# Kernel optimization log

Hardware: AMD Instinct MI355X
Metric: run time of the kernel (lower is better)

## Reference

```python
import jax, jax.numpy as jnp
import numpy as np

B, T, M, VM = 64, 512, 8, 50  # batch, time, num_modules, rois per module
EPS = 1e-5  # BatchNorm eps


def setup_inputs() -> dict:
    key = jax.random.key(0)
    ks = jax.random.split(key, 12)
    x = jax.random.normal(ks[0], (B, M * VM, T, 1), jnp.float32)
    # learned adjacency, torch init = ones/V; perturb slightly
    PA = jnp.full((M, VM, VM), 1.0 / VM, jnp.float32) + 0.01 * jax.random.normal(ks[1], (M, VM, VM), jnp.float32)
    conv_w = jax.random.normal(ks[2], (M,), jnp.float32)          # 1x1 conv weight (1->1 chan) per module
    conv_b = 0.1 * jax.random.normal(ks[3], (M,), jnp.float32)
    bn_gamma = 1.0 + 0.1 * jax.random.normal(ks[4], (M,), jnp.float32)
    bn_beta = 0.1 * jax.random.normal(ks[5], (M,), jnp.float32)
    bn_mean = 0.1 * jax.random.normal(ks[6], (M,), jnp.float32)
    bn_var = jax.random.uniform(ks[7], (M,), jnp.float32) + 0.5   # positive
    w1 = jax.random.normal(ks[8], (M, 8), jnp.float32) * 0.5      # Linear(1,8) weight per module
    b1 = 0.1 * jax.random.normal(ks[9], (M, 8), jnp.float32)
    w2 = jax.random.normal(ks[10], (M, 8), jnp.float32) * 0.5     # Linear(8,1) weight per module
    b2 = 0.1 * jax.random.normal(ks[11], (M,), jnp.float32)
    return dict(x=x, PA=PA, conv_w=conv_w, conv_b=conv_b, bn_gamma=bn_gamma, bn_beta=bn_beta,
                bn_mean=bn_mean, bn_var=bn_var, w1=w1, b1=b1, w2=w2, b2=b2)


def reference(x, PA, conv_w, conv_b, bn_gamma, bn_beta, bn_mean, bn_var, w1, b1, w2, b2):
    # x: [B, V_total, T, 1]; torch permute(0,3,2,1) -> [B, C=1, T, V_total]
    xp = x[..., 0].transpose(0, 2, 1)                 # [B, T, V_total]
    xm = xp.reshape(B, T, M, VM)                      # contiguous module blocks == index_select
    # UnitGCN: x_agg = x @ A per module
    agg = jnp.einsum('btmv,mvw->btmw', xm, PA)        # [B, T, M, VM]
    # 1x1 conv (scalar per module) + BatchNorm2d(1) in eval mode + ReLU
    y = agg * conv_w[:, None] + conv_b[:, None]
    scale = bn_gamma / jnp.sqrt(bn_var + EPS)
    h = jax.nn.relu((y - bn_mean[:, None]) * scale[:, None] + bn_beta[:, None])
    # AttentionPooling: MLP(1->8->1) on channel dim, softmax over nodes, weighted sum
    hid = jnp.tanh(h[..., None] * w1[:, None, :] + b1[:, None, :])   # [B, T, M, VM, 8]
    score = jnp.einsum('btmvh,mh->btmv', hid, w2) + b2[:, None]      # [B, T, M, VM]
    attn = jax.nn.softmax(score, axis=3)
    pooled = jnp.sum(h * attn, axis=3)                # [B, T, M]
    # concat over modules on dim 1 -> [B, M, T, 1]
    return pooled.transpose(0, 2, 1)[..., None]
```

## Files before the change

### kernel.cpp

```cpp
#include <hip/hip_runtime.h>

#define BB 64
#define TT 512
#define MM 8
#define VMM 50
#define TBLK 128
#define RSTRIDE 36
#define EPSV 1e-5f

#define TN   1024
#define HMAX 16.0f
#define HSTEP (HMAX / TN)
#define INVH  (TN / HMAX)

#define WS_GT(m)  ((m) * TN)
#define WS_PA(m)  (MM * TN + (m) * (64 * 32))
#define WS_NEED   ((MM * TN + MM * 64 * 32) * 4)

using short8  = __attribute__((ext_vector_type(8))) short;
using float4v = __attribute__((ext_vector_type(4))) float;

__device__ __forceinline__ float fast_rcp(float x) {
    return __builtin_amdgcn_rcpf(x);
}
__device__ __forceinline__ float fast_tanh(float x) {
    float e2 = __expf(2.0f * x);
    return fmaf(-2.0f, fast_rcp(e2 + 1.0f), 1.0f);
}
__device__ __forceinline__ unsigned f2bf(float f) {
    unsigned u = __float_as_uint(f);
    return (u + 0x7FFFu + ((u >> 16) & 1u)) >> 16;
}
__device__ __forceinline__ unsigned pack2(float lo, float hi) {
    return f2bf(lo) | (f2bf(hi) << 16);
}
__device__ __forceinline__ unsigned packh2(float lo, float hi) {
    unsigned short a = __builtin_bit_cast(unsigned short, (_Float16)lo);
    unsigned short b = __builtin_bit_cast(unsigned short, (_Float16)hi);
    return (unsigned)a | ((unsigned)b << 16);
}
__device__ __forceinline__ float h2f_lo(unsigned p) {
    return (float)__builtin_bit_cast(_Float16, (unsigned short)(p & 0xFFFFu));
}
__device__ __forceinline__ float h2f_hi(unsigned p) {
    return (float)__builtin_bit_cast(_Float16, (unsigned short)(p >> 16));
}

__global__ __launch_bounds__(256, 4)
void prep_kernel(const float* __restrict__ PA,
                 const float* __restrict__ w1,
                 const float* __restrict__ b1,
                 const float* __restrict__ w2,
                 const float* __restrict__ b2,
                 unsigned* __restrict__ ws)
{
    const int m = blockIdx.x;
    const int j = threadIdx.x;

    {
        float W1[8], B1[8], W2[8];
        float B2 = b2[m], sabs = 0.0f;
#pragma unroll
        for (int k = 0; k < 8; ++k) {
            W1[k] = w1[m * 8 + k];
            B1[k] = b1[m * 8 + k];
            W2[k] = w2[m * 8 + k];
            sabs += fabsf(W2[k]);
        }
        const float s0 = (B2 + sabs) - 8.0f;
        float gv[5];
#pragma unroll
        for (int k = 0; k < 5; ++k) {
            float h = (4 * j + k) * HSTEP;
            float s = B2 - s0;
#pragma unroll
            for (int i = 0; i < 8; ++i)
                s = fmaf(W2[i], fast_tanh(fmaf(h, W1[i], B1[i])), s);
            gv[k] = __expf(s);
        }
#pragma unroll
        for (int k = 0; k < 4; ++k)
            ws[WS_GT(m) + 4 * j + k] = packh2(gv[k], gv[k + 1] - gv[k]);
    }

    {
        const float* pa = PA + m * (VMM * VMM);
        const int w  = j & 63;
        const int vb = (j >> 6) * 8;
#pragma unroll
        for (int i = 0; i < 8; ++i) {
            int vp = vb + i, v0 = 2 * vp, v1 = v0 + 1;
            float a = (w < VMM && v0 < VMM) ? pa[v0 * VMM + w] : 0.0f;
            float c = (w < VMM && v1 < VMM) ? pa[v1 * VMM + w] : 0.0f;
            ws[WS_PA(m) + w * 32 + vp] = pack2(a, c);
        }
    }
}

__global__ __launch_bounds__(256, 4)
void intra_module_agg_kernel(const float* __restrict__ x,
                             const float* __restrict__ conv_w,
                             const float* __restrict__ conv_b,
                             const float* __restrict__ bn_gamma,
                             const float* __restrict__ bn_beta,
                             const float* __restrict__ bn_mean,
                             const float* __restrict__ bn_var,
                             const unsigned* __restrict__ ws,
                             float* __restrict__ out)
{
    const int blk = blockIdx.x;
    const int tq  = blk & 3;
    const int m   = (blk >> 2) & 7;
    const int b   = blk >> 5;
    const int j   = threadIdx.x;

    __shared__ __align__(16) unsigned xsu[TBLK * RSTRIDE];
    __shared__ __align__(16) unsigned psu[64 * RSTRIDE];
    __shared__ __align__(16) unsigned gt[TN];

    const float scale = bn_gamma[m] * __frsqrt_rn(bn_var[m] + EPSV);
    const float Amul  = conv_w[m] * scale;
    const float Cadd  = (conv_b[m] - bn_mean[m]) * scale + bn_beta[m];

    {
        uint4 g = ((const uint4*)(ws + WS_GT(m)))[j];
        *(uint4*)&gt[4 * j] = g;
    }
    {
        const uint4* src = (const uint4*)(ws + WS_PA(m));
#pragma unroll
        for (int p = 0; p < 2; ++p) {
            int i4 = j + p * 256;
            uint4 v = src[i4];
            int r = i4 >> 3;
            int c = (i4 & 7) * 4;
            *(uint4*)&psu[r * RSTRIDE + c] = v;
        }
    }

    {
        const int t  = j >> 1;
        const int hf = j & 1;
        const float* xb = x + ((b * (MM * VMM) + m * VMM) * TT + tq * TBLK + t);
        unsigned* row = &xsu[t * RSTRIDE];
        const int vp0 = hf * 13;
#pragma unroll
        for (int i = 0; i < 13; ++i) {
            int vp = vp0 + i;
            float a = 0.0f, c = 0.0f;
            if (vp < 25) { a = xb[(2 * vp) * TT]; c = xb[(2 * vp + 1) * TT]; }
            row[vp] = pack2(a, c);
        }
        if (hf) {
#pragma unroll
            for (int vp = 26; vp < 32; ++vp) row[vp] = 0u;
        }
    }

    __syncthreads();

    const int lane = j & 63, wv = j >> 6;
    const int q = lane >> 4, nl = lane & 15;

    short8 A[4][2];
#pragma unroll
    for (int wt = 0; wt < 4; ++wt)
#pragma unroll
        for (int ks = 0; ks < 2; ++ks)
            A[wt][ks] = *(const short8*)&psu[(wt * 16 + nl) * RSTRIDE + ks * 16 + q * 4];

    float4v C[2][4];
#pragma unroll
    for (int t2 = 0; t2 < 2; ++t2)
#pragma unroll
        for (int wt = 0; wt < 4; ++wt)
            C[t2][wt] = (float4v){0.f, 0.f, 0.f, 0.f};

#pragma unroll
    for (int t2 = 0; t2 < 2; ++t2) {
        const int trow = (wv * 2 + t2) * 16 + nl;
        short8 Bv0 = *(const short8*)&xsu[trow * RSTRIDE + 0 * 16 + q * 4];
        short8 Bv1 = *(const short8*)&xsu[trow * RSTRIDE + 1 * 16 + q * 4];
#pragma unroll
        for (int wt = 0; wt < 4; ++wt) {
            C[t2][wt] = __builtin_amdgcn_mfma_f32_16x16x32_bf16(A[wt][0], Bv0, C[t2][wt], 0, 0, 0);
            C[t2][wt] = __builtin_amdgcn_mfma_f32_16x16x32_bf16(A[wt][1], Bv1, C[t2][wt], 0, 0, 0);
        }
    }

    const int obase = (b * MM + m) * TT + tq * TBLK;
#pragma unroll
    for (int t2 = 0; t2 < 2; ++t2) {
        float se = 0.0f, sh = 0.0f;
#pragma unroll
        for (int wt = 0; wt < 4; ++wt) {
#pragma unroll
            for (int r = 0; r < 4; ++r) {
                const int w = wt * 16 + q * 4 + r;
                float h = fmaxf(fmaf(C[t2][wt][r], Amul, Cadd), 0.0f);
                float u = fminf(h, HMAX - 0.0005f) * INVH;
                int   i = (int)u;
                float fr = u - (float)i;
                unsigned p = gt[i];
                float e = (w < VMM) ? fmaf(fr, h2f_hi(p), h2f_lo(p)) : 0.0f;
                se += e;
                sh = fmaf(h, e, sh);
            }
        }
        se += __shfl_xor(se, 16, 64);
        se += __shfl_xor(se, 32, 64);
        sh += __shfl_xor(sh, 16, 64);
        sh += __shfl_xor(sh, 32, 64);
        if (q == 0)
            out[obase + (wv * 2 + t2) * 16 + nl] = sh * fast_rcp(se);
    }
}

__global__ __launch_bounds__(256, 4)
void mono_kernel(const float* __restrict__ x,
                 const float* __restrict__ PA,
                 const float* __restrict__ conv_w,
                 const float* __restrict__ conv_b,
                 const float* __restrict__ bn_gamma,
                 const float* __restrict__ bn_beta,
                 const float* __restrict__ bn_mean,
                 const float* __restrict__ bn_var,
                 const float* __restrict__ w1,
                 const float* __restrict__ b1,
                 const float* __restrict__ w2,
                 const float* __restrict__ b2,
                 float* __restrict__ out)
{
    const int blk = blockIdx.x;
    const int tq  = blk & 3;
    const int m   = (blk >> 2) & 7;
    const int b   = blk >> 5;
    const int j   = threadIdx.x;

    __shared__ __align__(16) unsigned xsu[TBLK * RSTRIDE];
    __shared__ __align__(16) unsigned psu[64 * RSTRIDE];
    __shared__ __align__(16) unsigned gt[TN];

    const float scale = bn_gamma[m] * __frsqrt_rn(bn_var[m] + EPSV);
    const float Amul  = conv_w[m] * scale;
    const float Cadd  = (conv_b[m] - bn_mean[m]) * scale + bn_beta[m];

    {
        const int t  = j >> 1;
        const int hf = j & 1;
        const float* xb = x + ((b * (MM * VMM) + m * VMM) * TT + tq * TBLK + t);
        unsigned* row = &xsu[t * RSTRIDE];
        const int vp0 = hf * 13;
#pragma unroll
        for (int i = 0; i < 13; ++i) {
            int vp = vp0 + i;
            float a = 0.0f, c = 0.0f;
            if (vp < 25) { a = xb[(2 * vp) * TT]; c = xb[(2 * vp + 1) * TT]; }
            row[vp] = pack2(a, c);
        }
        if (hf) {
#pragma unroll
            for (int vp = 26; vp < 32; ++vp) row[vp] = 0u;
        }
    }
    {
        const float* pa = PA + m * (VMM * VMM);
        const int w  = j & 63;
        const int vb = (j >> 6) * 8;
#pragma unroll
        for (int i = 0; i < 8; ++i) {
            int vp = vb + i, v0 = 2 * vp, v1 = v0 + 1;
            float a = (w < VMM && v0 < VMM) ? pa[v0 * VMM + w] : 0.0f;
            float c = (w < VMM && v1 < VMM) ? pa[v1 * VMM + w] : 0.0f;
            psu[w * RSTRIDE + vp] = pack2(a, c);
        }
    }
    {
        float W1[8], B1[8], W2[8];
        float B2 = b2[m], sabs = 0.0f;
#pragma unroll
        for (int k = 0; k < 8; ++k) {
            W1[k] = w1[m * 8 + k];
            B1[k] = b1[m * 8 + k];
            W2[k] = w2[m * 8 + k];
            sabs += fabsf(W2[k]);
        }
        const float s0 = (B2 + sabs) - 8.0f;
        float gv[5];
#pragma unroll
        for (int k = 0; k < 5; ++k) {
            float h = (4 * j + k) * HSTEP;
            float s = B2 - s0;
#pragma unroll
            for (int i = 0; i < 8; ++i)
                s = fmaf(W2[i], fast_tanh(fmaf(h, W1[i], B1[i])), s);
            gv[k] = __expf(s);
        }
#pragma unroll
        for (int k = 0; k < 4; ++k)
            gt[4 * j + k] = packh2(gv[k], gv[k + 1] - gv[k]);
    }

    __syncthreads();

    const int lane = j & 63, wv = j >> 6;
    const int q = lane >> 4, nl = lane & 15;

    short8 A[4][2];
#pragma unroll
    for (int wt = 0; wt < 4; ++wt)
#pragma unroll
        for (int ks = 0; ks < 2; ++ks)
            A[wt][ks] = *(const short8*)&psu[(wt * 16 + nl) * RSTRIDE + ks * 16 + q * 4];

    float4v C[2][4];
#pragma unroll
    for (int t2 = 0; t2 < 2; ++t2)
#pragma unroll
        for (int wt = 0; wt < 4; ++wt)
            C[t2][wt] = (float4v){0.f, 0.f, 0.f, 0.f};

#pragma unroll
    for (int t2 = 0; t2 < 2; ++t2) {
        const int trow = (wv * 2 + t2) * 16 + nl;
        short8 Bv0 = *(const short8*)&xsu[trow * RSTRIDE + 0 * 16 + q * 4];
        short8 Bv1 = *(const short8*)&xsu[trow * RSTRIDE + 1 * 16 + q * 4];
#pragma unroll
        for (int wt = 0; wt < 4; ++wt) {
            C[t2][wt] = __builtin_amdgcn_mfma_f32_16x16x32_bf16(A[wt][0], Bv0, C[t2][wt], 0, 0, 0);
            C[t2][wt] = __builtin_amdgcn_mfma_f32_16x16x32_bf16(A[wt][1], Bv1, C[t2][wt], 0, 0, 0);
        }
    }

    const int obase = (b * MM + m) * TT + tq * TBLK;
#pragma unroll
    for (int t2 = 0; t2 < 2; ++t2) {
        float se = 0.0f, sh = 0.0f;
#pragma unroll
        for (int wt = 0; wt < 4; ++wt) {
#pragma unroll
            for (int r = 0; r < 4; ++r) {
                const int w = wt * 16 + q * 4 + r;
                float h = fmaxf(fmaf(C[t2][wt][r], Amul, Cadd), 0.0f);
                float u = fminf(h, HMAX - 0.0005f) * INVH;
                int   i = (int)u;
                float fr = u - (float)i;
                unsigned p = gt[i];
                float e = (w < VMM) ? fmaf(fr, h2f_hi(p), h2f_lo(p)) : 0.0f;
                se += e;
                sh = fmaf(h, e, sh);
            }
        }
        se += __shfl_xor(se, 16, 64);
        se += __shfl_xor(se, 32, 64);
        sh += __shfl_xor(sh, 16, 64);
        sh += __shfl_xor(sh, 32, 64);
        if (q == 0)
            out[obase + (wv * 2 + t2) * 16 + nl] = sh * fast_rcp(se);
    }
}

extern "C" void kernel_launch(void* const* d_in, const int* in_sizes, int n_in,
                              void* d_out, int out_size, void* d_ws, size_t ws_size,
                              hipStream_t stream) {
    const float* x        = (const float*)d_in[0];
    const float* PA       = (const float*)d_in[1];
    const float* conv_w   = (const float*)d_in[2];
    const float* conv_b   = (const float*)d_in[3];
    const float* bn_gamma = (const float*)d_in[4];
    const float* bn_beta  = (const float*)d_in[5];
    const float* bn_mean  = (const float*)d_in[6];
    const float* bn_var   = (const float*)d_in[7];
    const float* w1       = (const float*)d_in[8];
    const float* b1       = (const float*)d_in[9];
    const float* w2       = (const float*)d_in[10];
    const float* b2       = (const float*)d_in[11];
    float* out = (float*)d_out;

    if (ws_size >= (size_t)WS_NEED) {
        unsigned* ws = (unsigned*)d_ws;
        prep_kernel<<<dim3(MM), dim3(256), 0, stream>>>(PA, w1, b1, w2, b2, ws);
        intra_module_agg_kernel<<<dim3(BB * MM * (TT / TBLK)), dim3(256), 0, stream>>>(
            x, conv_w, conv_b, bn_gamma, bn_beta, bn_mean, bn_var, ws, out);
    } else {
        mono_kernel<<<dim3(BB * MM * (TT / TBLK)), dim3(256), 0, stream>>>(
            x, PA, conv_w, conv_b, bn_gamma, bn_beta, bn_mean, bn_var,
            w1, b1, w2, b2, out);
    }
}
```

Before: 112.5 us.

## Load MFMA operands straight from global into registers, bypassing LDS staging

The prep kernel now stores the adjacency in MFMA-fragment order, so each lane fetches its A operand with coalesced uint4 loads from the workspace. Each lane also loads its own x values from global and packs them into bf16 B fragments in registers, which removes the shared-memory tiles for x and PA and the sync that sat before the MMA. The only barrier left guards the lookup table, and it now runs after the MFMAs. In exchange, the x loads become per-lane strided reads (each lane reads 16 values spaced TT apart), and register pressure goes up.

Result: faster. 108.1 us (-4.0%).

```diff
diff --git a/kernel.cpp b/kernel.cpp
--- a/kernel.cpp
+++ b/kernel.cpp
@@ -5,7 +5,6 @@
 #define MM 8
 #define VMM 50
 #define TBLK 128
-#define RSTRIDE 36
 #define EPSV 1e-5f
 
 #define TN   1024
@@ -13,9 +12,9 @@
 #define HSTEP (HMAX / TN)
 #define INVH  (TN / HMAX)
 
-#define WS_GT(m)  ((m) * TN)
-#define WS_PA(m)  (MM * TN + (m) * (64 * 32))
-#define WS_NEED   ((MM * TN + MM * 64 * 32) * 4)
+#define WS_GT(m)   ((m) * TN)
+#define WS_PAF(m)  (MM * TN + (m) * (8 * 64 * 4))
+#define WS_NEED    ((MM * TN + MM * 8 * 64 * 4) * 4)
 
 using short8  = __attribute__((ext_vector_type(8))) short;
 using float4v = __attribute__((ext_vector_type(4))) float;
@@ -85,14 +84,24 @@
 
     {
         const float* pa = PA + m * (VMM * VMM);
-        const int w  = j & 63;
-        const int vb = (j >> 6) * 8;
-#pragma unroll
-        for (int i = 0; i < 8; ++i) {
-            int vp = vb + i, v0 = 2 * vp, v1 = v0 + 1;
-            float a = (w < VMM && v0 < VMM) ? pa[v0 * VMM + w] : 0.0f;
-            float c = (w < VMM && v1 < VMM) ? pa[v1 * VMM + w] : 0.0f;
-            ws[WS_PA(m) + w * 32 + vp] = pack2(a, c);
+        uint4* dst = (uint4*)(ws + WS_PAF(m));
+#pragma unroll
+        for (int p = 0; p < 2; ++p) {
+            int id   = j + p * 256;
+            int wt   = id >> 7;
+            int ks   = (id >> 6) & 1;
+            int lane = id & 63;
+            int w    = wt * 16 + (lane & 15);
+            int vp0  = ks * 16 + (lane >> 4) * 4;
+            unsigned u[4];
+#pragma unroll
+            for (int k = 0; k < 4; ++k) {
+                int vp = vp0 + k, v0 = 2 * vp, v1 = v0 + 1;
+                float a = (w < VMM && v0 < VMM) ? pa[v0 * VMM + w] : 0.0f;
+                float c = (w < VMM && v1 < VMM) ? pa[v1 * VMM + w] : 0.0f;
+                u[k] = pack2(a, c);
+            }
+            dst[(wt * 2 + ks) * 64 + lane] = make_uint4(u[0], u[1], u[2], u[3]);
         }
     }
 }
@@ -114,60 +123,59 @@
     const int b   = blk >> 5;
     const int j   = threadIdx.x;
 
-    __shared__ __align__(16) unsigned xsu[TBLK * RSTRIDE];
-    __shared__ __align__(16) unsigned psu[64 * RSTRIDE];
+    const int lane = j & 63, wv = j >> 6;
+    const int q = lane >> 4, nl = lane & 15;
+
     __shared__ __align__(16) unsigned gt[TN];
 
     const float scale = bn_gamma[m] * __frsqrt_rn(bn_var[m] + EPSV);
     const float Amul  = conv_w[m] * scale;
     const float Cadd  = (conv_b[m] - bn_mean[m]) * scale + bn_beta[m];
 
-    {
-        uint4 g = ((const uint4*)(ws + WS_GT(m)))[j];
-        *(uint4*)&gt[4 * j] = g;
-    }
-    {
-        const uint4* src = (const uint4*)(ws + WS_PA(m));
-#pragma unroll
-        for (int p = 0; p < 2; ++p) {
-            int i4 = j + p * 256;
-            uint4 v = src[i4];
-            int r = i4 >> 3;
-            int c = (i4 & 7) * 4;
-            *(uint4*)&psu[r * RSTRIDE + c] = v;
-        }
-    }
-
-    {
-        const int t  = j >> 1;
-        const int hf = j & 1;
-        const float* xb = x + ((b * (MM * VMM) + m * VMM) * TT + tq * TBLK + t);
-        unsigned* row = &xsu[t * RSTRIDE];
-        const int vp0 = hf * 13;
-#pragma unroll
-        for (int i = 0; i < 13; ++i) {
-            int vp = vp0 + i;
-            float a = 0.0f, c = 0.0f;
-            if (vp < 25) { a = xb[(2 * vp) * TT]; c = xb[(2 * vp + 1) * TT]; }
-            row[vp] = pack2(a, c);
-        }
-        if (hf) {
-#pragma unroll
-            for (int vp = 26; vp < 32; ++vp) row[vp] = 0u;
-        }
-    }
-
-    __syncthreads();
-
-    const int lane = j & 63, wv = j >> 6;
-    const int q = lane >> 4, nl = lane & 15;
-
-    short8 A[4][2];
+    uint4 g = ((const uint4*)(ws + WS_GT(m)))[j];
+
+    const uint4* paf = (const uint4*)(ws + WS_PAF(m));
+    uint4 Araw[4][2];
 #pragma unroll
     for (int wt = 0; wt < 4; ++wt)
 #pragma unroll
         for (int ks = 0; ks < 2; ++ks)
-            A[wt][ks] = *(const short8*)&psu[(wt * 16 + nl) * RSTRIDE + ks * 16 + q * 4];
+            Araw[wt][ks] = paf[(wt * 2 + ks) * 64 + lane];
+
+    const int t0 = tq * TBLK;
+    float xr[2][16];
+#pragma unroll
+    for (int t2 = 0; t2 < 2; ++t2) {
+        const int t = t0 + (wv * 2 + t2) * 16 + nl;
+        const float* xg = x + ((b * (MM * VMM) + m * VMM) * TT + t);
+#pragma unroll
+        for (int jj = 0; jj < 8; ++jj) {
+            xr[t2][jj] = xg[(q * 8 + jj) * TT];
+        }
+#pragma unroll
+        for (int jj = 0; jj < 8; ++jj) {
+            int v  = 32 + q * 8 + jj;
+            int vc = (v < VMM) ? v : 0;
+            float tv = xg[vc * TT];
+            xr[t2][8 + jj] = (v < VMM) ? tv : 0.0f;
+        }
+    }
+
+    *(uint4*)&gt[4 * j] = g;
+
+    short8 Bf[2][2];
+#pragma unroll
+    for (int t2 = 0; t2 < 2; ++t2) {
+#pragma unroll
+        for (int ks = 0; ks < 2; ++ks) {
+            uint4 u;
+            u.x = pack2(xr[t2][8 * ks + 0], xr[t2][8 * ks + 1]);
+            u.y = pack2(xr[t2][8 * ks + 2], xr[t2][8 * ks + 3]);
+            u.z = pack2(xr[t2][8 * ks + 4], xr[t2][8 * ks + 5]);
+            u.w = pack2(xr[t2][8 * ks + 6], xr[t2][8 * ks + 7]);
+            Bf[t2][ks] = __builtin_bit_cast(short8, u);
+        }
+    }
 
     float4v C[2][4];
 #pragma unroll
@@ -178,17 +186,18 @@
 
 #pragma unroll
     for (int t2 = 0; t2 < 2; ++t2) {
-        const int trow = (wv * 2 + t2) * 16 + nl;
-        short8 Bv0 = *(const short8*)&xsu[trow * RSTRIDE + 0 * 16 + q * 4];
-        short8 Bv1 = *(const short8*)&xsu[trow * RSTRIDE + 1 * 16 + q * 4];
 #pragma unroll
         for (int wt = 0; wt < 4; ++wt) {
-            C[t2][wt] = __builtin_amdgcn_mfma_f32_16x16x32_bf16(A[wt][0], Bv0, C[t2][wt], 0, 0, 0);
-            C[t2][wt] = __builtin_amdgcn_mfma_f32_16x16x32_bf16(A[wt][1], Bv1, C[t2][wt], 0, 0, 0);
-        }
-    }
-
-    const int obase = (b * MM + m) * TT + tq * TBLK;
+            C[t2][wt] = __builtin_amdgcn_mfma_f32_16x16x32_bf16(
+                __builtin_bit_cast(short8, Araw[wt][0]), Bf[t2][0], C[t2][wt], 0, 0, 0);
+            C[t2][wt] = __builtin_amdgcn_mfma_f32_16x16x32_bf16(
+                __builtin_bit_cast(short8, Araw[wt][1]), Bf[t2][1], C[t2][wt], 0, 0, 0);
+        }
+    }
+
+    __syncthreads();
+
+    const int obase = (b * MM + m) * TT + t0;
 #pragma unroll
     for (int t2 = 0; t2 < 2; ++t2) {
         float se = 0.0f, sh = 0.0f;
@@ -216,6 +225,7 @@
     }
 }
 
+#define RSTRIDE 36
 __global__ __launch_bounds__(256, 4)
 void mono_kernel(const float* __restrict__ x,
                  const float* __restrict__ PA,
```
